# Optimization experiments

Hardware: AMD Instinct MI355X
Metric: run time of the kernel (lower is better)

Reference implementation:

```python
import jax, jax.numpy as jnp
import numpy as np

B, T, F, H, O = 8192, 10, 561, 256, 12


def _lstm_cell(x, h, c, Wih, Whh, bih, bhh):
    # PyTorch gate order: input, forget, cell(g), output
    gates = x @ Wih.T + bih + h @ Whh.T + bhh  # [B, 4H]
    i, f, g, o = jnp.split(gates, 4, axis=-1)
    c_new = jax.nn.sigmoid(f) * c + jax.nn.sigmoid(i) * jnp.tanh(g)
    h_new = jax.nn.sigmoid(o) * jnp.tanh(c_new)
    return h_new, c_new


def setup_inputs() -> dict:
    key = jax.random.key(0)
    ks = jax.random.split(key, 12)
    s_in = 1.0 / np.sqrt(F)
    s_h = 1.0 / np.sqrt(H)
    u = lambda k, shape, s: jax.random.uniform(k, shape, jnp.float32, -s, s)
    return {
        "inputs": jax.random.normal(ks[0], (B, T, F), jnp.float32),
        "W_inp": u(ks[1], (H, F), s_in), "b_inp": u(ks[2], (H,), s_in),
        "Wih0": u(ks[3], (4 * H, H), s_h), "Whh0": u(ks[4], (4 * H, H), s_h),
        "bih0": u(ks[5], (4 * H,), s_h), "bhh0": u(ks[6], (4 * H,), s_h),
        "Wih1": u(ks[7], (4 * H, H), s_h), "Whh1": u(ks[8], (4 * H, H), s_h),
        "bih1": u(ks[9], (4 * H,), s_h), "bhh1": u(ks[10], (4 * H,), s_h),
        "W_out": u(ks[11], (O, H), s_h), "b_out": jnp.zeros((O,), jnp.float32),
    }


def reference(inputs, W_inp, b_inp, Wih0, Whh0, bih0, bhh0,
              Wih1, Whh1, bih1, bhh1, W_out, b_out):
    b, t, _ = inputs.shape
    h = W_inp.shape[0]
    # input Linear applied to every timestep (same math as per-step self.inp)
    xp = jnp.einsum('btf,hf->bth', inputs, W_inp) + b_inp  # [B,T,H]

    def step(carry, x_t):
        h0, c0, h1, c1 = carry
        h0, c0 = _lstm_cell(x_t, h0, c0, Wih0, Whh0, bih0, bhh0)
        h1, c1 = _lstm_cell(h0, h1, c1, Wih1, Whh1, bih1, bhh1)
        return (h0, c0, h1, c1), h1

    z = jnp.zeros((b, h), inputs.dtype)
    (h0, c0, h1, c1), hs = jax.lax.scan(step, (z, z, z, z), jnp.swapaxes(xp, 0, 1))
    outputs = jnp.einsum('tbh,oh->bto', hs, W_out) + b_out  # [B,T,O]
    h_n = jnp.stack([h0, h1])  # [2,B,H] like torch LSTM hidden
    c_n = jnp.stack([c0, c1])
    return outputs, h_n, c_n
```

## Files before the change

### kernel.cpp

```cpp
#include <hip/hip_runtime.h>

#define BB 8192
#define TT 10
#define FF 561
#define FP 576
#define HH 256
#define OO 12

typedef __attribute__((ext_vector_type(8))) __bf16 bf16x8;
typedef __attribute__((ext_vector_type(4))) float f32x4;

__device__ __forceinline__ unsigned short f2bf(float f) {
  unsigned int u = __float_as_uint(f);
  u += 0x7fffu + ((u >> 16) & 1u);
  return (unsigned short)(u >> 16);
}
__device__ __forceinline__ float sigm(float x) { return 1.f / (1.f + __expf(-x)); }
__device__ __forceinline__ float tanh_fast(float x) { return 1.f - 2.f / (__expf(2.f * x) + 1.f); }

__device__ __forceinline__ void gl_lds16(const unsigned short* g, unsigned short* l) {
  __builtin_amdgcn_global_load_lds(
      (const __attribute__((address_space(1))) unsigned int*)g,
      (__attribute__((address_space(3))) unsigned int*)l, 16, 0, 0);
}

__device__ __forceinline__ void mfma_tile(const unsigned short* as, const unsigned short* bs,
                                          int w, int quad, int l15, f32x4 (&acc)[2][8]) {
  bf16x8 af[2], bfr[8];
#pragma unroll
  for (int mt = 0; mt < 2; ++mt)
    af[mt] = *(const bf16x8*)&as[(w * 32 + mt * 16 + l15) * 32 + quad * 8];
#pragma unroll
  for (int nt = 0; nt < 8; ++nt)
    bfr[nt] = *(const bf16x8*)&bs[(nt * 16 + l15) * 32 + quad * 8];
#pragma unroll
  for (int mt = 0; mt < 2; ++mt)
#pragma unroll
    for (int nt = 0; nt < 8; ++nt)
      acc[mt][nt] = __builtin_amdgcn_mfma_f32_16x16x32_bf16(af[mt], bfr[nt], acc[mt][nt], 0, 0, 0);
}

__global__ void conv_inputs(const float* __restrict__ in, unsigned short* __restrict__ Ain) {
  int idx = blockIdx.x * 256 + threadIdx.x;
  if (idx >= 81920 * 144) return;
  int c4 = (idx % 144) * 4;
  size_t row = idx / 144;
  const float* src = in + row * 561 + c4;
  ushort4 v;
  v.x = f2bf(c4 + 0 < 561 ? src[0] : 0.f);
  v.y = f2bf(c4 + 1 < 561 ? src[1] : 0.f);
  v.z = f2bf(c4 + 2 < 561 ? src[2] : 0.f);
  v.w = f2bf(c4 + 3 < 561 ? src[3] : 0.f);
  *(ushort4*)(Ain + row * 576 + c4) = v;
}

__global__ void conv_weights(const float* __restrict__ Winp,
                             const float* __restrict__ Wih0, const float* __restrict__ Whh0,
                             const float* __restrict__ Wih1, const float* __restrict__ Whh1,
                             const float* __restrict__ Wout,
                             unsigned short* __restrict__ Wib,
                             unsigned short* __restrict__ W0p,
                             unsigned short* __restrict__ W1p,
                             unsigned short* __restrict__ Wob) {
  int idx = blockIdx.x * 256 + threadIdx.x;
  if (idx < 256 * 576) {
    int kk = idx % 576, n = idx / 576;
    Wib[idx] = f2bf(kk < 561 ? Winp[n * 561 + kk] : 0.f);
    return;
  }
  idx -= 256 * 576;
  if (idx < 1024 * 512) {
    int kk = idx % 512, np = idx / 512;
    int h = (np >> 7) * 32 + (np & 31), g = (np >> 5) & 3;
    int sr = g * 256 + h;
    float v = kk < 256 ? Wih0[sr * 256 + kk] : Whh0[sr * 256 + kk - 256];
    W0p[idx] = f2bf(v);
    return;
  }
  idx -= 1024 * 512;
  if (idx < 1024 * 512) {
    int kk = idx % 512, np = idx / 512;
    int h = (np >> 7) * 32 + (np & 31), g = (np >> 5) & 3;
    int sr = g * 256 + h;
    float v = kk < 256 ? Wih1[sr * 256 + kk] : Whh1[sr * 256 + kk - 256];
    W1p[idx] = f2bf(v);
    return;
  }
  idx -= 1024 * 512;
  if (idx < 16 * 256) {
    int kk = idx % 256, o = idx / 256;
    Wob[idx] = f2bf(o < OO ? Wout[o * 256 + kk] : 0.f);
  }
}

__global__ __launch_bounds__(256, 2) void gemm_xp(
    const unsigned short* __restrict__ A, const unsigned short* __restrict__ W,
    const float* __restrict__ bias, unsigned short* __restrict__ xp) {
  __shared__ __align__(16) unsigned short As[2][128 * 32];
  __shared__ __align__(16) unsigned short Bs[2][128 * 32];
  const int tid = threadIdx.x;
  const int w = tid >> 6, lane = tid & 63, quad = lane >> 4, l15 = lane & 15;
  const int flat = blockIdx.x;
  const int xcd = flat & 7, kb = flat >> 3;
  const int nb = kb & 1, mb = xcd * 80 + (kb >> 1);
  const int r0 = tid >> 2, cc = (tid & 3) * 8;

  auto stage = [&](int buf, int k0) {
    gl_lds16(A + (size_t)(mb * 128 + r0) * FP + k0 + cc, &As[buf][tid * 8]);
    gl_lds16(A + (size_t)(mb * 128 + 64 + r0) * FP + k0 + cc, &As[buf][2048 + tid * 8]);
    gl_lds16(W + (size_t)(nb * 128 + r0) * FP + k0 + cc, &Bs[buf][tid * 8]);
    gl_lds16(W + (size_t)(nb * 128 + 64 + r0) * FP + k0 + cc, &Bs[buf][2048 + tid * 8]);
  };

  f32x4 acc[2][8];
#pragma unroll
  for (int i = 0; i < 2; ++i)
#pragma unroll
    for (int j = 0; j < 8; ++j) acc[i][j] = (f32x4){0.f, 0.f, 0.f, 0.f};

  stage(0, 0);
  __syncthreads();
  int cur = 0;
#pragma unroll
  for (int ks = 0; ks < 17; ++ks) {
    stage(cur ^ 1, (ks + 1) * 32);
    mfma_tile(&As[cur][0], &Bs[cur][0], w, quad, l15, acc);
    __syncthreads();
    cur ^= 1;
  }
  mfma_tile(&As[cur][0], &Bs[cur][0], w, quad, l15, acc);

#pragma unroll
  for (int mt = 0; mt < 2; ++mt) {
    int rowb = mb * 128 + w * 32 + mt * 16 + quad * 4;
#pragma unroll
    for (int nt = 0; nt < 8; ++nt) {
      int col = nb * 128 + nt * 16 + l15;
      float bv = bias[col];
#pragma unroll
      for (int r = 0; r < 4; ++r)
        xp[(size_t)(rowb + r) * HH + col] = f2bf(acc[mt][nt][r] + bv);
    }
  }
}

struct LstmJob {
  const unsigned short* A0; int lda0;
  const unsigned short* A1;
  const unsigned short* W;
  const float* bA; const float* bB;
  float* cbuf;
  unsigned short* hout;
  float* hf32; float* cf32;
};

__global__ __launch_bounds__(256, 2) void lstm_step(LstmJob j0, LstmJob j1, int njobs) {
  __shared__ __align__(16) unsigned short As[2][128 * 32];
  __shared__ __align__(16) unsigned short Bs[2][128 * 32];
  const int tid = threadIdx.x;
  const int w = tid >> 6, lane = tid & 63, quad = lane >> 4, l15 = lane & 15;
  const int flat = blockIdx.x;
  const int xcd = flat & 7, kb = flat >> 3;
  const int nb = kb >> 3, mb = xcd * 8 + (kb & 7);
  const int r0 = tid >> 2, cc = (tid & 3) * 8;

  auto stage = [&](const LstmJob& J, int buf, int k0) {
    const unsigned short* Asrc; int ldA, kk;
    if (k0 < 256) { Asrc = J.A0; ldA = J.lda0; kk = k0; }
    else          { Asrc = J.A1; ldA = HH;     kk = k0 - 256; }
    gl_lds16(Asrc + (size_t)(mb * 128 + r0) * ldA + kk + cc, &As[buf][tid * 8]);
    gl_lds16(Asrc + (size_t)(mb * 128 + 64 + r0) * ldA + kk + cc, &As[buf][2048 + tid * 8]);
    gl_lds16(J.W + (size_t)(nb * 128 + r0) * 512 + k0 + cc, &Bs[buf][tid * 8]);
    gl_lds16(J.W + (size_t)(nb * 128 + 64 + r0) * 512 + k0 + cc, &Bs[buf][2048 + tid * 8]);
  };

  stage(j0, 0, 0);

  for (int job = 0; job < njobs; ++job) {
    const LstmJob J = job ? j1 : j0;
    f32x4 acc[2][8];
#pragma unroll
    for (int i = 0; i < 2; ++i)
#pragma unroll
      for (int j = 0; j < 8; ++j) acc[i][j] = (f32x4){0.f, 0.f, 0.f, 0.f};

    __syncthreads();
    int cur = 0;
#pragma unroll
    for (int ks = 0; ks < 15; ++ks) {
      stage(J, cur ^ 1, (ks + 1) * 32);
      mfma_tile(&As[cur][0], &Bs[cur][0], w, quad, l15, acc);
      __syncthreads();
      cur ^= 1;
    }
    mfma_tile(&As[cur][0], &Bs[cur][0], w, quad, l15, acc);

    if (job + 1 < njobs) stage(j1, 0, 0);

#pragma unroll
    for (int hb = 0; hb < 2; ++hb) {
      const int hg = nb * 32 + hb * 16 + l15;
      const float bI = J.bA[hg] + J.bB[hg];
      const float bF = J.bA[256 + hg] + J.bB[256 + hg];
      const float bG = J.bA[512 + hg] + J.bB[512 + hg];
      const float bO = J.bA[768 + hg] + J.bB[768 + hg];
#pragma unroll
      for (int mt = 0; mt < 2; ++mt) {
        const int rowb = mb * 128 + w * 32 + mt * 16 + quad * 4;
#pragma unroll
        for (int r = 0; r < 4; ++r) {
          const size_t idx = (size_t)(rowb + r) * HH + hg;
          const float xi = acc[mt][0 + hb][r] + bI;
          const float xf = acc[mt][2 + hb][r] + bF;
          const float xg = acc[mt][4 + hb][r] + bG;
          const float xo = acc[mt][6 + hb][r] + bO;
          const float c_old = J.cbuf[idx];
          const float cn = sigm(xf) * c_old + sigm(xi) * tanh_fast(xg);
          const float hn = sigm(xo) * tanh_fast(cn);
          J.cbuf[idx] = cn;
          J.hout[idx] = f2bf(hn);
          if (J.hf32) { J.hf32[idx] = hn; J.cf32[idx] = cn; }
        }
      }
    }
  }
}

__global__ __launch_bounds__(256) void out_gemm_mfma(
    const unsigned short* __restrict__ hs,
    const unsigned short* __restrict__ Wob,
    const float* __restrict__ bout,
    float* __restrict__ out) {
  const int tid = threadIdx.x;
  const int w = tid >> 6, lane = tid & 63, quad = lane >> 4, l15 = lane & 15;
  const int m0 = blockIdx.x * 64 + w * 16;
  const unsigned short* arow = hs + (size_t)(m0 + l15 + BB) * HH + quad * 8;
  const unsigned short* brow = Wob + l15 * HH + quad * 8;
  f32x4 acc = (f32x4){0.f, 0.f, 0.f, 0.f};
#pragma unroll
  for (int k0 = 0; k0 < 8; ++k0) {
    bf16x8 a = *(const bf16x8*)(arow + k0 * 32);
    bf16x8 b = *(const bf16x8*)(brow + k0 * 32);
    acc = __builtin_amdgcn_mfma_f32_16x16x32_bf16(a, b, acc, 0, 0, 0);
  }
  const int o = l15;
  if (o < OO) {
    float bv = bout[o];
#pragma unroll
    for (int r = 0; r < 4; ++r) {
      int m = m0 + quad * 4 + r;
      int b = m & (BB - 1);
      int t = m >> 13;
      out[((size_t)b * TT + t) * OO + o] = acc[r] + bv;
    }
  }
}

extern "C" void kernel_launch(void* const* d_in, const int* in_sizes, int n_in,
                              void* d_out, int out_size, void* d_ws, size_t ws_size,
                              hipStream_t stream) {
  const float* inputs = (const float*)d_in[0];
  const float* W_inp  = (const float*)d_in[1];
  const float* b_inp  = (const float*)d_in[2];
  const float* Wih0   = (const float*)d_in[3];
  const float* Whh0   = (const float*)d_in[4];
  const float* bih0   = (const float*)d_in[5];
  const float* bhh0   = (const float*)d_in[6];
  const float* Wih1   = (const float*)d_in[7];
  const float* Whh1   = (const float*)d_in[8];
  const float* bih1   = (const float*)d_in[9];
  const float* bhh1   = (const float*)d_in[10];
  const float* W_out  = (const float*)d_in[11];
  const float* b_out  = (const float*)d_in[12];
  float* out = (float*)d_out;

  char* ws = (char*)d_ws;
  size_t off = 0;
  auto alloc = [&](size_t bytes) {
    char* p = ws + off;
    off += (bytes + 255) & ~(size_t)255;
    return p;
  };
  unsigned short* Ain = (unsigned short*)alloc((size_t)81920 * FP * 2);
  unsigned short* xp  = (unsigned short*)alloc((size_t)81920 * HH * 2);
  unsigned short* Wib = (unsigned short*)alloc((size_t)256 * FP * 2);
  unsigned short* W0p = (unsigned short*)alloc((size_t)1024 * 512 * 2);
  unsigned short* W1p = (unsigned short*)alloc((size_t)1024 * 512 * 2);
  unsigned short* Wob = (unsigned short*)alloc((size_t)16 * HH * 2);
  unsigned short* h0s = (unsigned short*)alloc((size_t)2 * BB * HH * 2);
  unsigned short* hs  = (unsigned short*)alloc((size_t)(TT + 1) * BB * HH * 2);
  float* c0 = (float*)alloc((size_t)BB * HH * 4);
  float* c1 = (float*)alloc((size_t)BB * HH * 4);

  hipMemsetAsync(h0s, 0, (size_t)BB * HH * 2, stream);
  hipMemsetAsync(hs, 0, (size_t)BB * HH * 2, stream);
  hipMemsetAsync(c0, 0, (size_t)BB * HH * 4, stream);
  hipMemsetAsync(c1, 0, (size_t)BB * HH * 4, stream);

  conv_inputs<<<(81920 * 144 + 255) / 256, 256, 0, stream>>>(inputs, Ain);
  {
    int nthr = 256 * 576 + 2 * 1024 * 512 + 16 * 256;
    conv_weights<<<(nthr + 255) / 256, 256, 0, stream>>>(W_inp, Wih0, Whh0, Wih1, Whh1,
                                                         W_out, Wib, W0p, W1p, Wob);
  }

  gemm_xp<<<1280, 256, 0, stream>>>(Ain, Wib, b_inp, xp);

  float* hn_out = out + (size_t)BB * TT * OO;
  float* cn_out = hn_out + (size_t)2 * BB * HH;

  for (int s = 0; s <= TT; ++s) {
    LstmJob jobs[2];
    int nj = 0;
    if (s < TT) {
      int t = s;
      jobs[nj++] = LstmJob{
          xp + (size_t)t * HH, TT * HH,
          h0s + (size_t)(t & 1) * BB * HH,
          W0p, bih0, bhh0, c0,
          h0s + (size_t)((t + 1) & 1) * BB * HH,
          (t == TT - 1) ? hn_out : nullptr,
          (t == TT - 1) ? cn_out : nullptr};
    }
    if (s > 0) {
      int t = s - 1;
      jobs[nj++] = LstmJob{
          h0s + (size_t)((t + 1) & 1) * BB * HH, HH,
          hs + (size_t)t * BB * HH,
          W1p, bih1, bhh1, c1,
          hs + (size_t)(t + 1) * BB * HH,
          (t == TT - 1) ? hn_out + (size_t)BB * HH : nullptr,
          (t == TT - 1) ? cn_out + (size_t)BB * HH : nullptr};
    }
    lstm_step<<<512, 256, 0, stream>>>(jobs[0], nj == 2 ? jobs[1] : jobs[0], nj);
  }

  out_gemm_mfma<<<1280, 256, 0, stream>>>(hs, Wob, b_out, out);
}
```

Measured before the change: 780.5 us.

## Fuse LSTM timesteps into a persistent kernel with per-row-block flag sync

Replaces the 11 per-step lstm_step launches with one persistent kernel. Each block loops over all timesteps, keeps both cell states in LDS instead of global memory, and syncs only with the 8 blocks sharing its batch rows through an atomic counter between layer 0 and layer 1. Layer 1 reorders its K loop so the h1prev half is loaded before the wait finishes. This removes launch gaps and c-state global traffic, but it relies on all 512 blocks being co-resident. LDS use grows by 32KB per block, which may cut occupancy and risks deadlock, bounded only by a timeout.

Measured after the change: 1.896 ms. +142.9%, slower.

```diff
diff --git a/kernel.cpp b/kernel.cpp
--- a/kernel.cpp
+++ b/kernel.cpp
@@ -144,85 +144,150 @@
   }
 }
 
-struct LstmJob {
-  const unsigned short* A0; int lda0;
-  const unsigned short* A1;
-  const unsigned short* W;
-  const float* bA; const float* bB;
-  float* cbuf;
-  unsigned short* hout;
-  float* hf32; float* cf32;
+struct PArgs {
+  const unsigned short* xp;
+  unsigned short* h0s;
+  unsigned short* hs;
+  const unsigned short* W0p;
+  const unsigned short* W1p;
+  const float *bih0, *bhh0, *bih1, *bhh1;
+  float* hn;
+  float* cn;
+  unsigned int* flags;
 };
 
-__global__ __launch_bounds__(256, 2) void lstm_step(LstmJob j0, LstmJob j1, int njobs) {
+__global__ __launch_bounds__(256, 2) void lstm_persist(PArgs p) {
   __shared__ __align__(16) unsigned short As[2][128 * 32];
   __shared__ __align__(16) unsigned short Bs[2][128 * 32];
+  __shared__ float c0l[128 * 32];
+  __shared__ float c1l[128 * 32];
   const int tid = threadIdx.x;
   const int w = tid >> 6, lane = tid & 63, quad = lane >> 4, l15 = lane & 15;
   const int flat = blockIdx.x;
-  const int xcd = flat & 7, kb = flat >> 3;
-  const int nb = kb >> 3, mb = xcd * 8 + (kb & 7);
+  const int nb = flat & 7, mb = flat >> 3;
   const int r0 = tid >> 2, cc = (tid & 3) * 8;
-
-  auto stage = [&](const LstmJob& J, int buf, int k0) {
-    const unsigned short* Asrc; int ldA, kk;
-    if (k0 < 256) { Asrc = J.A0; ldA = J.lda0; kk = k0; }
-    else          { Asrc = J.A1; ldA = HH;     kk = k0 - 256; }
-    gl_lds16(Asrc + (size_t)(mb * 128 + r0) * ldA + kk + cc, &As[buf][tid * 8]);
-    gl_lds16(Asrc + (size_t)(mb * 128 + 64 + r0) * ldA + kk + cc, &As[buf][2048 + tid * 8]);
-    gl_lds16(J.W + (size_t)(nb * 128 + r0) * 512 + k0 + cc, &Bs[buf][tid * 8]);
-    gl_lds16(J.W + (size_t)(nb * 128 + 64 + r0) * 512 + k0 + cc, &Bs[buf][2048 + tid * 8]);
-  };
-
-  stage(j0, 0, 0);
-
-  for (int job = 0; job < njobs; ++job) {
-    const LstmJob J = job ? j1 : j0;
-    f32x4 acc[2][8];
-#pragma unroll
-    for (int i = 0; i < 2; ++i)
-#pragma unroll
-      for (int j = 0; j < 8; ++j) acc[i][j] = (f32x4){0.f, 0.f, 0.f, 0.f};
-
-    __syncthreads();
-    int cur = 0;
-#pragma unroll
-    for (int ks = 0; ks < 15; ++ks) {
-      stage(J, cur ^ 1, (ks + 1) * 32);
-      mfma_tile(&As[cur][0], &Bs[cur][0], w, quad, l15, acc);
-      __syncthreads();
-      cur ^= 1;
-    }
-    mfma_tile(&As[cur][0], &Bs[cur][0], w, quad, l15, acc);
-
-    if (job + 1 < njobs) stage(j1, 0, 0);
-
+  unsigned int* flag = p.flags + mb * 64;
+
+  for (int i = tid; i < 128 * 32; i += 256) { c0l[i] = 0.f; c1l[i] = 0.f; }
+
+  auto stageA = [&](const unsigned short* src, int ld, int kk, int buf) {
+    gl_lds16(src + (size_t)(mb * 128 + r0) * ld + kk + cc, &As[buf][tid * 8]);
+    gl_lds16(src + (size_t)(mb * 128 + 64 + r0) * ld + kk + cc, &As[buf][2048 + tid * 8]);
+  };
+  auto stageB = [&](const unsigned short* W, int k0, int buf) {
+    gl_lds16(W + (size_t)(nb * 128 + r0) * 512 + k0 + cc, &Bs[buf][tid * 8]);
+    gl_lds16(W + (size_t)(nb * 128 + 64 + r0) * 512 + k0 + cc, &Bs[buf][2048 + tid * 8]);
+  };
+
+  auto epilogue = [&](f32x4 (&acc)[2][8], const float* bA, const float* bB,
+                      float* cl, unsigned short* hout, float* hf, float* cf) {
 #pragma unroll
     for (int hb = 0; hb < 2; ++hb) {
       const int hg = nb * 32 + hb * 16 + l15;
-      const float bI = J.bA[hg] + J.bB[hg];
-      const float bF = J.bA[256 + hg] + J.bB[256 + hg];
-      const float bG = J.bA[512 + hg] + J.bB[512 + hg];
-      const float bO = J.bA[768 + hg] + J.bB[768 + hg];
+      const float bI = bA[hg] + bB[hg];
+      const float bF = bA[256 + hg] + bB[256 + hg];
+      const float bG = bA[512 + hg] + bB[512 + hg];
+      const float bO = bA[768 + hg] + bB[768 + hg];
 #pragma unroll
       for (int mt = 0; mt < 2; ++mt) {
-        const int rowb = mb * 128 + w * 32 + mt * 16 + quad * 4;
+        const int rl = w * 32 + mt * 16 + quad * 4;
 #pragma unroll
         for (int r = 0; r < 4; ++r) {
-          const size_t idx = (size_t)(rowb + r) * HH + hg;
+          const int lidx = (rl + r) * 32 + hb * 16 + l15;
+          const size_t gidx = (size_t)(mb * 128 + rl + r) * HH + hg;
           const float xi = acc[mt][0 + hb][r] + bI;
           const float xf = acc[mt][2 + hb][r] + bF;
           const float xg = acc[mt][4 + hb][r] + bG;
           const float xo = acc[mt][6 + hb][r] + bO;
-          const float c_old = J.cbuf[idx];
-          const float cn = sigm(xf) * c_old + sigm(xi) * tanh_fast(xg);
-          const float hn = sigm(xo) * tanh_fast(cn);
-          J.cbuf[idx] = cn;
-          J.hout[idx] = f2bf(hn);
-          if (J.hf32) { J.hf32[idx] = hn; J.cf32[idx] = cn; }
+          const float c_old = cl[lidx];
+          const float cnv = sigm(xf) * c_old + sigm(xi) * tanh_fast(xg);
+          const float hnv = sigm(xo) * tanh_fast(cnv);
+          cl[lidx] = cnv;
+          hout[gidx] = f2bf(hnv);
+          if (hf) { hf[gidx] = hnv; cf[gidx] = cnv; }
         }
       }
     }
+  };
+
+  stageA(p.xp, TT * HH, 0, 0);
+  stageB(p.W0p, 0, 0);
+
+  unsigned int target = 0;
+  for (int t = 0; t < TT; ++t) {
+    const unsigned short* xpt = p.xp + (size_t)t * HH;
+    const unsigned short* h0prev = p.h0s + (size_t)(t & 1) * BB * HH;
+    unsigned short* h0new = p.h0s + (size_t)((t + 1) & 1) * BB * HH;
+    const unsigned short* h1prev = p.hs + (size_t)t * BB * HH;
+    unsigned short* h1new = p.hs + (size_t)(t + 1) * BB * HH;
+    const bool last = (t == TT - 1);
+
+    f32x4 acc[2][8];
+#pragma unroll
+    for (int i = 0; i < 2; ++i)
+#pragma unroll
+      for (int j = 0; j < 8; ++j) acc[i][j] = (f32x4){0.f, 0.f, 0.f, 0.f};
+
+    __syncthreads();
+    int cur = 0;
+#pragma unroll
+    for (int ks = 0; ks < 15; ++ks) {
+      const int k0 = (ks + 1) * 32;
+      if (k0 < 256) stageA(xpt, TT * HH, k0, cur ^ 1);
+      else          stageA(h0prev, HH, k0 - 256, cur ^ 1);
+      stageB(p.W0p, k0, cur ^ 1);
+      mfma_tile(&As[cur][0], &Bs[cur][0], w, quad, l15, acc);
+      __syncthreads();
+      cur ^= 1;
+    }
+    mfma_tile(&As[cur][0], &Bs[cur][0], w, quad, l15, acc);
+    stageB(p.W1p, 256, 0);
+
+    epilogue(acc, p.bih0, p.bhh0, c0l, h0new,
+             last ? p.hn : nullptr, last ? p.cn : nullptr);
+
+    __threadfence();
+    __syncthreads();
+    ++target;
+    if (tid == 0) {
+      __hip_atomic_fetch_add(flag, 1u, __ATOMIC_RELEASE, __HIP_MEMORY_SCOPE_AGENT);
+      long long spin0 = (long long)clock64();
+      while (__hip_atomic_load(flag, __ATOMIC_ACQUIRE, __HIP_MEMORY_SCOPE_AGENT) < 8u * target) {
+        __builtin_amdgcn_s_sleep(2);
+        if ((long long)clock64() - spin0 > 100000000LL) break;
+      }
+    }
+    __syncthreads();
+    __threadfence();
+
+#pragma unroll
+    for (int i = 0; i < 2; ++i)
+#pragma unroll
+      for (int j = 0; j < 8; ++j) acc[i][j] = (f32x4){0.f, 0.f, 0.f, 0.f};
+
+    stageA(h1prev, HH, 0, 0);
+    __syncthreads();
+    cur = 0;
+#pragma unroll
+    for (int ls = 0; ls < 15; ++ls) {
+      const int ks = (ls + 9) & 15;
+      const int k0 = ks * 32;
+      if (ks >= 8) stageA(h1prev, HH, k0 - 256, cur ^ 1);
+      else         stageA(h0new, HH, k0, cur ^ 1);
+      stageB(p.W1p, k0, cur ^ 1);
+      mfma_tile(&As[cur][0], &Bs[cur][0], w, quad, l15, acc);
+      __syncthreads();
+      cur ^= 1;
+    }
+    mfma_tile(&As[cur][0], &Bs[cur][0], w, quad, l15, acc);
+    if (t + 1 < TT) {
+      stageA(p.xp + (size_t)(t + 1) * HH, TT * HH, 0, 0);
+      stageB(p.W0p, 0, 0);
+    }
+
+    epilogue(acc, p.bih1, p.bhh1, c1l, h1new,
+             last ? p.hn + (size_t)BB * HH : nullptr,
+             last ? p.cn + (size_t)BB * HH : nullptr);
   }
 }
 
@@ -289,13 +354,11 @@
   unsigned short* Wob = (unsigned short*)alloc((size_t)16 * HH * 2);
   unsigned short* h0s = (unsigned short*)alloc((size_t)2 * BB * HH * 2);
   unsigned short* hs  = (unsigned short*)alloc((size_t)(TT + 1) * BB * HH * 2);
-  float* c0 = (float*)alloc((size_t)BB * HH * 4);
-  float* c1 = (float*)alloc((size_t)BB * HH * 4);
+  unsigned int* flags = (unsigned int*)alloc((size_t)64 * 64 * 4);
 
   hipMemsetAsync(h0s, 0, (size_t)BB * HH * 2, stream);
   hipMemsetAsync(hs, 0, (size_t)BB * HH * 2, stream);
-  hipMemsetAsync(c0, 0, (size_t)BB * HH * 4, stream);
-  hipMemsetAsync(c1, 0, (size_t)BB * HH * 4, stream);
+  hipMemsetAsync(flags, 0, (size_t)64 * 64 * 4, stream);
 
   conv_inputs<<<(81920 * 144 + 255) / 256, 256, 0, stream>>>(inputs, Ain);
   {
@@ -309,31 +372,13 @@
   float* hn_out = out + (size_t)BB * TT * OO;
   float* cn_out = hn_out + (size_t)2 * BB * HH;
 
-  for (int s = 0; s <= TT; ++s) {
-    LstmJob jobs[2];
-    int nj = 0;
-    if (s < TT) {
-      int t = s;
-      jobs[nj++] = LstmJob{
-          xp + (size_t)t * HH, TT * HH,
-          h0s + (size_t)(t & 1) * BB * HH,
-          W0p, bih0, bhh0, c0,
-          h0s + (size_t)((t + 1) & 1) * BB * HH,
-          (t == TT - 1) ? hn_out : nullptr,
-          (t == TT - 1) ? cn_out : nullptr};
-    }
-    if (s > 0) {
-      int t = s - 1;
-      jobs[nj++] = LstmJob{
-          h0s + (size_t)((t + 1) & 1) * BB * HH, HH,
-          hs + (size_t)t * BB * HH,
-          W1p, bih1, bhh1, c1,
-          hs + (size_t)(t + 1) * BB * HH,
-          (t == TT - 1) ? hn_out + (size_t)BB * HH : nullptr,
-          (t == TT - 1) ? cn_out + (size_t)BB * HH : nullptr};
-    }
-    lstm_step<<<512, 256, 0, stream>>>(jobs[0], nj == 2 ? jobs[1] : jobs[0], nj);
-  }
+  PArgs pa;
+  pa.xp = xp; pa.h0s = h0s; pa.hs = hs;
+  pa.W0p = W0p; pa.W1p = W1p;
+  pa.bih0 = bih0; pa.bhh0 = bhh0; pa.bih1 = bih1; pa.bhh1 = bhh1;
+  pa.hn = hn_out; pa.cn = cn_out;
+  pa.flags = flags;
+  lstm_persist<<<512, 256, 0, stream>>>(pa);
 
   out_gemm_mfma<<<1280, 256, 0, stream>>>(hs, Wob, b_out, out);
 }
```

## Fuse all LSTM timesteps into one persistent row-blocked kernel

Applied to the files above, without the earlier changes.

Replaces the 11 per-timestep lstm_step launches with a single lstm_rows kernel. Each block owns 32 batch rows for all timesteps and both layers, keeping h in LDS and c in registers, and streams weights straight from global/L2 into MFMA operands. This removes launch overhead, the global round-trips of h and c state, and the memsets. In exchange each block rereads the full 2 MB of weights every step without LDS staging, and only 256 blocks at occupancy 1 run, which may leave MFMA units underfed.

Measured after the change: 1.230 ms. 1.58x slower.

```diff
diff --git a/kernel.cpp b/kernel.cpp
--- a/kernel.cpp
+++ b/kernel.cpp
@@ -58,10 +58,13 @@
                              const float* __restrict__ Wih0, const float* __restrict__ Whh0,
                              const float* __restrict__ Wih1, const float* __restrict__ Whh1,
                              const float* __restrict__ Wout,
+                             const float* __restrict__ bih0, const float* __restrict__ bhh0,
+                             const float* __restrict__ bih1, const float* __restrict__ bhh1,
                              unsigned short* __restrict__ Wib,
                              unsigned short* __restrict__ W0p,
                              unsigned short* __restrict__ W1p,
-                             unsigned short* __restrict__ Wob) {
+                             unsigned short* __restrict__ Wob,
+                             float* __restrict__ bc0, float* __restrict__ bc1) {
   int idx = blockIdx.x * 256 + threadIdx.x;
   if (idx < 256 * 576) {
     int kk = idx % 576, n = idx / 576;
@@ -90,7 +93,12 @@
   if (idx < 16 * 256) {
     int kk = idx % 256, o = idx / 256;
     Wob[idx] = f2bf(o < OO ? Wout[o * 256 + kk] : 0.f);
-  }
+    return;
+  }
+  idx -= 16 * 256;
+  if (idx < 1024) { bc0[idx] = bih0[idx] + bhh0[idx]; return; }
+  idx -= 1024;
+  if (idx < 1024) { bc1[idx] = bih1[idx] + bhh1[idx]; }
 }
 
 __global__ __launch_bounds__(256, 2) void gemm_xp(
@@ -144,85 +152,136 @@
   }
 }
 
-struct LstmJob {
-  const unsigned short* A0; int lda0;
-  const unsigned short* A1;
-  const unsigned short* W;
-  const float* bA; const float* bB;
-  float* cbuf;
-  unsigned short* hout;
-  float* hf32; float* cf32;
+struct RArgs {
+  const unsigned short* xp;
+  unsigned short* hs;
+  const unsigned short* W0p;
+  const unsigned short* W1p;
+  const float* bc0;
+  const float* bc1;
+  float* hn;
+  float* cn;
 };
 
-__global__ __launch_bounds__(256, 2) void lstm_step(LstmJob j0, LstmJob j1, int njobs) {
-  __shared__ __align__(16) unsigned short As[2][128 * 32];
-  __shared__ __align__(16) unsigned short Bs[2][128 * 32];
+__global__ __launch_bounds__(256, 1) void lstm_rows(RArgs p) {
+  __shared__ __align__(16) unsigned short h0l[32 * 264];
+  __shared__ __align__(16) unsigned short h1l[32 * 264];
   const int tid = threadIdx.x;
-  const int w = tid >> 6, lane = tid & 63, quad = lane >> 4, l15 = lane & 15;
-  const int flat = blockIdx.x;
-  const int xcd = flat & 7, kb = flat >> 3;
-  const int nb = kb >> 3, mb = xcd * 8 + (kb & 7);
-  const int r0 = tid >> 2, cc = (tid & 3) * 8;
-
-  auto stage = [&](const LstmJob& J, int buf, int k0) {
-    const unsigned short* Asrc; int ldA, kk;
-    if (k0 < 256) { Asrc = J.A0; ldA = J.lda0; kk = k0; }
-    else          { Asrc = J.A1; ldA = HH;     kk = k0 - 256; }
-    gl_lds16(Asrc + (size_t)(mb * 128 + r0) * ldA + kk + cc, &As[buf][tid * 8]);
-    gl_lds16(Asrc + (size_t)(mb * 128 + 64 + r0) * ldA + kk + cc, &As[buf][2048 + tid * 8]);
-    gl_lds16(J.W + (size_t)(nb * 128 + r0) * 512 + k0 + cc, &Bs[buf][tid * 8]);
-    gl_lds16(J.W + (size_t)(nb * 128 + 64 + r0) * 512 + k0 + cc, &Bs[buf][2048 + tid * 8]);
-  };
-
-  stage(j0, 0, 0);
-
-  for (int job = 0; job < njobs; ++job) {
-    const LstmJob J = job ? j1 : j0;
-    f32x4 acc[2][8];
+  const int w = tid >> 6, lane = tid & 63, q4 = lane >> 4, l15 = lane & 15;
+  const int b0 = blockIdx.x * 32;
+
+  for (int i = tid; i < 32 * 264; i += 256) { h0l[i] = 0; h1l[i] = 0; }
+
+  f32x4 c0r[2][2][2], c1r[2][2][2];
+#pragma unroll
+  for (int a = 0; a < 2; ++a)
+#pragma unroll
+    for (int b = 0; b < 2; ++b)
+#pragma unroll
+      for (int c = 0; c < 2; ++c) {
+        c0r[a][b][c] = (f32x4){0.f, 0.f, 0.f, 0.f};
+        c1r[a][b][c] = (f32x4){0.f, 0.f, 0.f, 0.f};
+      }
+
+  f32x4 acc[2][16];
+  const int bofs = (w * 256 + l15) * 512 + q4 * 8;
+
+  auto zacc = [&]() {
 #pragma unroll
     for (int i = 0; i < 2; ++i)
 #pragma unroll
-      for (int j = 0; j < 8; ++j) acc[i][j] = (f32x4){0.f, 0.f, 0.f, 0.f};
-
-    __syncthreads();
-    int cur = 0;
-#pragma unroll
-    for (int ks = 0; ks < 15; ++ks) {
-      stage(J, cur ^ 1, (ks + 1) * 32);
-      mfma_tile(&As[cur][0], &Bs[cur][0], w, quad, l15, acc);
-      __syncthreads();
-      cur ^= 1;
-    }
-    mfma_tile(&As[cur][0], &Bs[cur][0], w, quad, l15, acc);
-
-    if (job + 1 < njobs) stage(j1, 0, 0);
-
-#pragma unroll
-    for (int hb = 0; hb < 2; ++hb) {
-      const int hg = nb * 32 + hb * 16 + l15;
-      const float bI = J.bA[hg] + J.bB[hg];
-      const float bF = J.bA[256 + hg] + J.bB[256 + hg];
-      const float bG = J.bA[512 + hg] + J.bB[512 + hg];
-      const float bO = J.bA[768 + hg] + J.bB[768 + hg];
-#pragma unroll
-      for (int mt = 0; mt < 2; ++mt) {
-        const int rowb = mb * 128 + w * 32 + mt * 16 + quad * 4;
-#pragma unroll
-        for (int r = 0; r < 4; ++r) {
-          const size_t idx = (size_t)(rowb + r) * HH + hg;
-          const float xi = acc[mt][0 + hb][r] + bI;
-          const float xf = acc[mt][2 + hb][r] + bF;
-          const float xg = acc[mt][4 + hb][r] + bG;
-          const float xo = acc[mt][6 + hb][r] + bO;
-          const float c_old = J.cbuf[idx];
-          const float cn = sigm(xf) * c_old + sigm(xi) * tanh_fast(xg);
-          const float hn = sigm(xo) * tanh_fast(cn);
-          J.cbuf[idx] = cn;
-          J.hout[idx] = f2bf(hn);
-          if (J.hf32) { J.hf32[idx] = hn; J.cf32[idx] = cn; }
-        }
+      for (int j = 0; j < 16; ++j) acc[i][j] = (f32x4){0.f, 0.f, 0.f, 0.f};
+  };
+
+  auto khalf_glob = [&](const unsigned short* abase, const unsigned short* Wh) {
+    const unsigned short* a0 = abase + (size_t)l15 * (TT * HH) + q4 * 8;
+    const unsigned short* a1 = abase + (size_t)(16 + l15) * (TT * HH) + q4 * 8;
+    const unsigned short* bW = Wh + bofs;
+#pragma unroll 4
+    for (int ks = 0; ks < 8; ++ks) {
+      bf16x8 af0 = __builtin_nontemporal_load((const bf16x8*)(a0 + ks * 32));
+      bf16x8 af1 = __builtin_nontemporal_load((const bf16x8*)(a1 + ks * 32));
+#pragma unroll
+      for (int nf = 0; nf < 16; ++nf) {
+        bf16x8 bf = *(const bf16x8*)(bW + nf * 8192 + ks * 32);
+        acc[0][nf] = __builtin_amdgcn_mfma_f32_16x16x32_bf16(af0, bf, acc[0][nf], 0, 0, 0);
+        acc[1][nf] = __builtin_amdgcn_mfma_f32_16x16x32_bf16(af1, bf, acc[1][nf], 0, 0, 0);
       }
     }
+  };
+
+  auto khalf_lds = [&](const unsigned short* hl, const unsigned short* Wh) {
+    const unsigned short* a0 = hl + l15 * 264 + q4 * 8;
+    const unsigned short* a1 = hl + (16 + l15) * 264 + q4 * 8;
+    const unsigned short* bW = Wh + bofs;
+#pragma unroll 4
+    for (int ks = 0; ks < 8; ++ks) {
+      bf16x8 af0 = *(const bf16x8*)(a0 + ks * 32);
+      bf16x8 af1 = *(const bf16x8*)(a1 + ks * 32);
+#pragma unroll
+      for (int nf = 0; nf < 16; ++nf) {
+        bf16x8 bf = *(const bf16x8*)(bW + nf * 8192 + ks * 32);
+        acc[0][nf] = __builtin_amdgcn_mfma_f32_16x16x32_bf16(af0, bf, acc[0][nf], 0, 0, 0);
+        acc[1][nf] = __builtin_amdgcn_mfma_f32_16x16x32_bf16(af1, bf, acc[1][nf], 0, 0, 0);
+      }
+    }
+  };
+
+  auto cell = [&](f32x4 (&cr)[2][2][2], const float* bc, unsigned short* hl,
+                  unsigned short* hg, float* hf, float* cf) {
+#pragma unroll
+    for (int mt = 0; mt < 2; ++mt)
+#pragma unroll
+      for (int hi2 = 0; hi2 < 2; ++hi2)
+#pragma unroll
+        for (int lo = 0; lo < 2; ++lo) {
+          const int hcol = w * 64 + hi2 * 32 + lo * 16 + l15;
+          const float bI = bc[hcol];
+          const float bF = bc[256 + hcol];
+          const float bG = bc[512 + hcol];
+          const float bO = bc[768 + hcol];
+          const f32x4& xi = acc[mt][hi2 * 8 + 0 + lo];
+          const f32x4& xf = acc[mt][hi2 * 8 + 2 + lo];
+          const f32x4& xg = acc[mt][hi2 * 8 + 4 + lo];
+          const f32x4& xo = acc[mt][hi2 * 8 + 6 + lo];
+#pragma unroll
+          for (int r = 0; r < 4; ++r) {
+            const int row = mt * 16 + q4 * 4 + r;
+            const float co = cr[mt][hi2][lo][r];
+            const float cnv = sigm(xf[r] + bF) * co + sigm(xi[r] + bI) * tanh_fast(xg[r] + bG);
+            const float hnv = sigm(xo[r] + bO) * tanh_fast(cnv);
+            cr[mt][hi2][lo][r] = cnv;
+            hl[row * 264 + hcol] = f2bf(hnv);
+            if (hg) __builtin_nontemporal_store(f2bf(hnv), hg + (size_t)row * HH + hcol);
+            if (hf) {
+              hf[(size_t)row * HH + hcol] = hnv;
+              cf[(size_t)row * HH + hcol] = cnv;
+            }
+          }
+        }
+  };
+
+  __syncthreads();
+
+  for (int t = 0; t < TT; ++t) {
+    const bool last = (t == TT - 1);
+    zacc();
+    khalf_glob(p.xp + (size_t)b0 * (TT * HH) + t * HH, p.W0p);
+    khalf_lds(h0l, p.W0p + 256);
+    __syncthreads();
+    cell(c0r, p.bc0, h0l, nullptr,
+         last ? p.hn + (size_t)b0 * HH : nullptr,
+         last ? p.cn + (size_t)b0 * HH : nullptr);
+    __syncthreads();
+    zacc();
+    khalf_lds(h0l, p.W1p);
+    khalf_lds(h1l, p.W1p + 256);
+    __syncthreads();
+    cell(c1r, p.bc1, h1l,
+         p.hs + (size_t)(t + 1) * BB * HH + (size_t)b0 * HH,
+         last ? p.hn + (size_t)BB * HH + (size_t)b0 * HH : nullptr,
+         last ? p.cn + (size_t)BB * HH + (size_t)b0 * HH : nullptr);
+    __syncthreads();
   }
 }
 
@@ -287,21 +346,16 @@
   unsigned short* W0p = (unsigned short*)alloc((size_t)1024 * 512 * 2);
   unsigned short* W1p = (unsigned short*)alloc((size_t)1024 * 512 * 2);
   unsigned short* Wob = (unsigned short*)alloc((size_t)16 * HH * 2);
-  unsigned short* h0s = (unsigned short*)alloc((size_t)2 * BB * HH * 2);
   unsigned short* hs  = (unsigned short*)alloc((size_t)(TT + 1) * BB * HH * 2);
-  float* c0 = (float*)alloc((size_t)BB * HH * 4);
-  float* c1 = (float*)alloc((size_t)BB * HH * 4);
-
-  hipMemsetAsync(h0s, 0, (size_t)BB * HH * 2, stream);
-  hipMemsetAsync(hs, 0, (size_t)BB * HH * 2, stream);
-  hipMemsetAsync(c0, 0, (size_t)BB * HH * 4, stream);
-  hipMemsetAsync(c1, 0, (size_t)BB * HH * 4, stream);
+  float* bc0 = (float*)alloc((size_t)1024 * 4);
+  float* bc1 = (float*)alloc((size_t)1024 * 4);
 
   conv_inputs<<<(81920 * 144 + 255) / 256, 256, 0, stream>>>(inputs, Ain);
   {
-    int nthr = 256 * 576 + 2 * 1024 * 512 + 16 * 256;
-    conv_weights<<<(nthr + 255) / 256, 256, 0, stream>>>(W_inp, Wih0, Whh0, Wih1, Whh1,
-                                                         W_out, Wib, W0p, W1p, Wob);
+    int nthr = 256 * 576 + 2 * 1024 * 512 + 16 * 256 + 2048;
+    conv_weights<<<(nthr + 255) / 256, 256, 0, stream>>>(
+        W_inp, Wih0, Whh0, Wih1, Whh1, W_out, bih0, bhh0, bih1, bhh1,
+        Wib, W0p, W1p, Wob, bc0, bc1);
   }
 
   gemm_xp<<<1280, 256, 0, stream>>>(Ain, Wib, b_inp, xp);
@@ -309,31 +363,12 @@
   float* hn_out = out + (size_t)BB * TT * OO;
   float* cn_out = hn_out + (size_t)2 * BB * HH;
 
-  for (int s = 0; s <= TT; ++s) {
-    LstmJob jobs[2];
-    int nj = 0;
-    if (s < TT) {
-      int t = s;
-      jobs[nj++] = LstmJob{
-          xp + (size_t)t * HH, TT * HH,
-          h0s + (size_t)(t & 1) * BB * HH,
-          W0p, bih0, bhh0, c0,
-          h0s + (size_t)((t + 1) & 1) * BB * HH,
-          (t == TT - 1) ? hn_out : nullptr,
-          (t == TT - 1) ? cn_out : nullptr};
-    }
-    if (s > 0) {
-      int t = s - 1;
-      jobs[nj++] = LstmJob{
-          h0s + (size_t)((t + 1) & 1) * BB * HH, HH,
-          hs + (size_t)t * BB * HH,
-          W1p, bih1, bhh1, c1,
-          hs + (size_t)(t + 1) * BB * HH,
-          (t == TT - 1) ? hn_out + (size_t)BB * HH : nullptr,
-          (t == TT - 1) ? cn_out + (size_t)BB * HH : nullptr};
-    }
-    lstm_step<<<512, 256, 0, stream>>>(jobs[0], nj == 2 ? jobs[1] : jobs[0], nj);
-  }
+  RArgs ra;
+  ra.xp = xp; ra.hs = hs;
+  ra.W0p = W0p; ra.W1p = W1p;
+  ra.bc0 = bc0; ra.bc1 = bc1;
+  ra.hn = hn_out; ra.cn = cn_out;
+  lstm_rows<<<256, 256, 0, stream>>>(ra);
 
   out_gemm_mfma<<<1280, 256, 0, stream>>>(hs, Wob, b_out, out);
 }
```
